# Kernel optimization log

Measured on AMD Instinct MI355X. Metric: run time of the kernel, lower is better.

## Reference

```python
import jax, jax.numpy as jnp
import numpy as np
import math

B, L, D, E, H = 8, 128, 512, 64, 8
SLOPE = 0.2
EPS = 1e-5


def setup_inputs() -> dict:
    key = jax.random.key(0)
    ks = jax.random.split(key, 10)
    s = 0.02
    x = jax.random.normal(ks[0], (B, L, D), jnp.float32)
    adj = jax.random.randint(ks[1], (B, L, L), 0, 2, jnp.int32)  # 0/1 adjacency
    e = jax.random.normal(ks[2], (B, L, L, E), jnp.float32)
    Wq = jax.random.normal(ks[3], (D, D), jnp.float32) * s
    Wkv = jax.random.normal(ks[4], (D, D), jnp.float32) * s
    We = jax.random.normal(ks[5], (E, D), jnp.float32) * s
    Wf = jax.random.normal(ks[6], (D, D), jnp.float32) * s
    bf = jnp.zeros((D,), jnp.float32)
    gamma = jnp.ones((D,), jnp.float32)
    beta = jnp.zeros((D,), jnp.float32)
    return {"x": x, "adj": adj, "e": e, "Wq": Wq, "Wkv": Wkv, "We": We,
            "Wf": Wf, "bf": bf, "gamma": gamma, "beta": beta}


def reference(x, adj, e, Wq, Wkv, We, Wf, bf, gamma, beta):
    C = D // H
    # projections
    q = (x @ Wq).reshape(B, L, H, C).transpose(0, 2, 1, 3)    # (B,H,L,C)
    kv = (x @ Wkv).reshape(B, L, H, C).transpose(0, 2, 1, 3)  # (B,H,L,C)
    ee = (e @ We).reshape(B, L, L, H, C).transpose(0, 3, 1, 2, 4)  # (B,H,Lq,Lk,C)
    # edge-modulated value/key: depends on both query and key position
    kve = kv[:, :, None, :, :] + ee                            # (B,H,Lq,Lk,C)
    # scores
    alpha = jnp.einsum('bhqc,bhqkc->bhqk', q, kve) / math.sqrt(C)
    alpha = jax.nn.leaky_relu(alpha, SLOPE)
    mask = (adj != 0)[:, None, :, :]                           # (B,1,Lq,Lk)
    alpha = jnp.where(mask, alpha, jnp.float32(-1e9))
    alpha = jax.nn.softmax(alpha, axis=-1)                     # over keys
    # weighted sum of edge-modulated values
    out = jnp.einsum('bhqk,bhqkc->bhqc', alpha, kve)           # (B,H,L,C)
    out = out.transpose(0, 2, 1, 3).reshape(B, L, D)
    # FFN: Linear -> LayerNorm -> ReLU
    out = out @ Wf + bf
    mu = out.mean(-1, keepdims=True)
    var = ((out - mu) ** 2).mean(-1, keepdims=True)
    out = (out - mu) / jnp.sqrt(var + EPS) * gamma + beta
    return jax.nn.relu(out)
```

## Files before the change

kernel.cpp:

```cpp
#include <hip/hip_runtime.h>
#include <hip/hip_bf16.h>
#include <math.h>

#define BB 8
#define LL 128
#define DD 512
#define EE 64
#define HH 8
#define CC 64
#define SLOPE 0.2f
#define EPS 1e-5f

typedef short bf16x8v __attribute__((ext_vector_type(8)));
typedef float f32x4v __attribute__((ext_vector_type(4)));

static __device__ __forceinline__ unsigned short f2bf(float f) {
    union { float f; unsigned u; } v; v.f = f;
    unsigned r = v.u + 0x7FFFu + ((v.u >> 16) & 1u);
    return (unsigned short)(r >> 16);
}

static __device__ __forceinline__ bf16x8v ld8f_bf(const float* __restrict__ p) {
    const float4 v0 = *(const float4*)p;
    const float4 v1 = *(const float4*)(p + 4);
    bf16x8v r;
    r[0] = (short)f2bf(v0.x); r[1] = (short)f2bf(v0.y);
    r[2] = (short)f2bf(v0.z); r[3] = (short)f2bf(v0.w);
    r[4] = (short)f2bf(v1.x); r[5] = (short)f2bf(v1.y);
    r[6] = (short)f2bf(v1.z); r[7] = (short)f2bf(v1.w);
    return r;
}

__global__ __launch_bounds__(256) void pack_all(
    const float* __restrict__ x, const float* __restrict__ Wq,
    const float* __restrict__ Wkv, const float* __restrict__ Wf,
    const float* __restrict__ We,
    unsigned short* __restrict__ xb, unsigned short* __restrict__ Wqkv_t,
    unsigned short* __restrict__ Wf_t, unsigned short* __restrict__ We_bf,
    unsigned short* __restrict__ WeT_bf)
{
    const int blk = blockIdx.x, tid = threadIdx.x;
    if (blk < 256) {
        const int j = blk * 512 + tid * 2;
        #pragma unroll
        for (int i = 0; i < 2; ++i) {
            const float4 v = ((const float4*)x)[j + i];
            ushort4 u; u.x = f2bf(v.x); u.y = f2bf(v.y); u.z = f2bf(v.z); u.w = f2bf(v.w);
            ((ushort4*)xb)[j + i] = u;
        }
    } else if (blk < 1024) {
        __shared__ float tile[32][33];
        const int matId = (blk - 256) >> 8;
        const int t = (blk - 256) & 255;
        const float* src = matId == 0 ? Wq : (matId == 1 ? Wkv : Wf);
        unsigned short* dst = matId == 0 ? Wqkv_t : (matId == 1 ? Wqkv_t + DD * DD : Wf_t);
        const int xx = tid & 31, yy = tid >> 5;
        const int r0 = (t >> 4) * 32, c0 = (t & 15) * 32;
        #pragma unroll
        for (int j = 0; j < 32; j += 8)
            tile[yy + j][xx] = src[(r0 + yy + j) * DD + c0 + xx];
        __syncthreads();
        #pragma unroll
        for (int j = 0; j < 32; j += 8)
            dst[(c0 + yy + j) * DD + r0 + xx] = f2bf(tile[xx][yy + j]);
    } else if (blk < 1040) {
        const int j = (blk - 1024) * 512 + tid * 2;
        #pragma unroll
        for (int i = 0; i < 2; ++i) {
            const float4 v = ((const float4*)We)[j + i];
            ushort4 u; u.x = f2bf(v.x); u.y = f2bf(v.y); u.z = f2bf(v.z); u.w = f2bf(v.w);
            ((ushort4*)We_bf)[j + i] = u;
        }
    } else if (blk < 1072) {
        __shared__ float tile[32][33];
        const int t = blk - 1040;
        const int xx = tid & 31, yy = tid >> 5;
        const int r0 = (t >> 4) * 32, c0 = (t & 15) * 32;
        #pragma unroll
        for (int j = 0; j < 32; j += 8)
            tile[yy + j][xx] = We[(r0 + yy + j) * DD + c0 + xx];
        __syncthreads();
        #pragma unroll
        for (int j = 0; j < 32; j += 8)
            WeT_bf[(c0 + yy + j) * EE + r0 + xx] = f2bf(tile[xx][yy + j]);
    } else {
        const int blk2 = blk - 1072;
        const int h = blk2 >> 3;
        const int d0 = (blk2 & 7) * 64;
        const int wave = tid >> 6, lane = tid & 63;
        const int quad = lane >> 4, l16 = lane & 15;
        const int dr = d0 + wave * 16;
        f32x4v acc[4];
        #pragma unroll
        for (int t = 0; t < 4; ++t) acc[t] = (f32x4v){0.f,0.f,0.f,0.f};
        #pragma unroll
        for (int ks = 0; ks < 2; ++ks) {
            const bf16x8v a = ld8f_bf(Wq + (dr + l16) * DD + h * CC + quad * 8 + ks * 32);
            #pragma unroll
            for (int t = 0; t < 4; ++t) {
                const bf16x8v bb = ld8f_bf(We + (t * 16 + l16) * DD + h * CC + quad * 8 + ks * 32);
                acc[t] = __builtin_amdgcn_mfma_f32_16x16x32_bf16(a, bb, acc[t], 0, 0, 0);
            }
        }
        #pragma unroll
        for (int t = 0; t < 4; ++t) {
            const int nrow = 1024 + h * CC + t * 16 + l16;
            #pragma unroll
            for (int r = 0; r < 4; ++r)
                Wqkv_t[nrow * DD + dr + quad * 4 + r] = f2bf(acc[t][r]);
        }
    }
}

__global__ __launch_bounds__(256) void proj_gemm(
    const unsigned short* __restrict__ A, const unsigned short* __restrict__ Bm,
    unsigned short* __restrict__ Q_bf, unsigned short* __restrict__ KV_bf,
    unsigned short* __restrict__ KVT_bf, unsigned short* __restrict__ T_bf)
{
    const int wave = threadIdx.x >> 6, lane = threadIdx.x & 63;
    const int quad = lane >> 4, l16 = lane & 15;
    const int m0 = blockIdx.y * 64 + wave * 16;
    const int n0 = blockIdx.x * 64;
    const bf16x8v* Ap = (const bf16x8v*)(A + (m0 + l16) * DD) + quad;
    const bf16x8v* Bp = (const bf16x8v*)(Bm + (n0 + l16) * DD) + quad;
    f32x4v acc0 = {0.f,0.f,0.f,0.f}, acc1 = acc0, acc2 = acc0, acc3 = acc0;
    #pragma unroll 4
    for (int k = 0; k < 16; ++k) {
        const bf16x8v a = Ap[k * 4];
        acc0 = __builtin_amdgcn_mfma_f32_16x16x32_bf16(a, Bp[k * 4       ], acc0, 0, 0, 0);
        acc1 = __builtin_amdgcn_mfma_f32_16x16x32_bf16(a, Bp[k * 4 + 1024], acc1, 0, 0, 0);
        acc2 = __builtin_amdgcn_mfma_f32_16x16x32_bf16(a, Bp[k * 4 + 2048], acc2, 0, 0, 0);
        acc3 = __builtin_amdgcn_mfma_f32_16x16x32_bf16(a, Bp[k * 4 + 3072], acc3, 0, 0, 0);
    }
    const f32x4v accs[4] = {acc0, acc1, acc2, acc3};
    const int gm0 = m0 + quad * 4;
    #pragma unroll
    for (int t = 0; t < 4; ++t) {
        const int gn = n0 + t * 16 + l16;
        const int mat = gn >> 9, d = gn & 511, h = d >> 6, c = d & 63;
        ushort4 pk;
        pk.x = f2bf(accs[t][0]); pk.y = f2bf(accs[t][1]);
        pk.z = f2bf(accs[t][2]); pk.w = f2bf(accs[t][3]);
        unsigned short* dst = mat == 0 ? Q_bf : (mat == 1 ? KV_bf : T_bf);
        dst[(gm0 + 0) * DD + d] = pk.x;
        dst[(gm0 + 1) * DD + d] = pk.y;
        dst[(gm0 + 2) * DD + d] = pk.z;
        dst[(gm0 + 3) * DD + d] = pk.w;
        if (mat == 1) {
            const int b = gm0 >> 7, l0 = gm0 & 127;
            *(ushort4*)&KVT_bf[(((b * HH + h) * CC + c) << 7) + l0] = pk;
        }
    }
}

__global__ __launch_bounds__(256) void qk_s1(
    const unsigned short* __restrict__ Q_bf, const unsigned short* __restrict__ KV_bf,
    float* __restrict__ S1)
{
    const int wave = threadIdx.x >> 6, lane = threadIdx.x & 63;
    const int quad = lane >> 4, l16 = lane & 15;
    const int bid = blockIdx.x;
    const int batch = bid >> 3;
    const int sub = bid & 7;
    const int b = batch >> 3, h = batch & 7;
    const int q0 = (sub >> 1) * 32 + (wave >> 1) * 16;
    const int k0 = (sub & 1) * 64 + (wave & 1) * 32;
    f32x4v acc[2];
    acc[0] = (f32x4v){0.f,0.f,0.f,0.f}; acc[1] = acc[0];
    const unsigned short* Ap = Q_bf + (b * LL + q0 + l16) * DD + h * CC + quad * 8;
    #pragma unroll
    for (int ks = 0; ks < 2; ++ks) {
        const bf16x8v a = *(const bf16x8v*)(Ap + ks * 32);
        #pragma unroll
        for (int t = 0; t < 2; ++t) {
            const bf16x8v bb = *(const bf16x8v*)(KV_bf + (b * LL + k0 + t * 16 + l16) * DD + h * CC + quad * 8 + ks * 32);
            acc[t] = __builtin_amdgcn_mfma_f32_16x16x32_bf16(a, bb, acc[t], 0, 0, 0);
        }
    }
    #pragma unroll
    for (int t = 0; t < 2; ++t)
        #pragma unroll
        for (int r = 0; r < 4; ++r)
            S1[((batch * LL + q0 + quad * 4 + r) << 7) + k0 + t * 16 + l16] = acc[t][r];
}

#define ES 72
#define ETS 138
__global__ __launch_bounds__(256) void attn_fused(
    const float* __restrict__ e, const int* __restrict__ adj,
    const float* __restrict__ S1, const unsigned short* __restrict__ T_bf,
    unsigned short* __restrict__ P1, unsigned short* __restrict__ G_bf)
{
    __shared__ unsigned short lds_e[LL * ES];
    __shared__ unsigned short lds_eT[EE * ETS];
    __shared__ float s_lds[HH * 132];
    __shared__ unsigned short p_bf[HH * ETS];

    const int bq = blockIdx.x;
    const int b = bq >> 7, q = bq & 127;
    const int tid = threadIdx.x;
    const int wave = tid >> 6, lane = tid & 63, quad = lane >> 4, l16 = lane & 15;

    const float4* e4 = (const float4*)(e + (size_t)bq * (LL * EE));
    #pragma unroll
    for (int rep = 0; rep < 8; ++rep) {
        const int j = rep * 256 + tid;
        const float4 v = e4[j];
        const int k = j >> 4, x0 = (j & 15) * 4;
        ushort4 u; u.x = f2bf(v.x); u.y = f2bf(v.y); u.z = f2bf(v.z); u.w = f2bf(v.w);
        *(ushort4*)&lds_e[k * ES + x0] = u;
        lds_eT[(x0    ) * ETS + k] = u.x;
        lds_eT[(x0 + 1) * ETS + k] = u.y;
        lds_eT[(x0 + 2) * ETS + k] = u.z;
        lds_eT[(x0 + 3) * ETS + k] = u.w;
    }
    __syncthreads();

    const int hh = l16 < 8 ? l16 : 7;
    const unsigned short* Trow = T_bf + bq * DD + hh * CC + quad * 8;
    const bf16x8v tb0 = *(const bf16x8v*)(Trow);
    const bf16x8v tb1 = *(const bf16x8v*)(Trow + 32);
    f32x4v sacc[2];
    #pragma unroll
    for (int mt = 0; mt < 2; ++mt) {
        sacc[mt] = (f32x4v){0.f,0.f,0.f,0.f};
        const int kb = wave * 32 + mt * 16;
        const bf16x8v a0 = *(const bf16x8v*)&lds_e[(kb + l16) * ES + quad * 8];
        const bf16x8v a1 = *(const bf16x8v*)&lds_e[(kb + l16) * ES + 32 + quad * 8];
        sacc[mt] = __builtin_amdgcn_mfma_f32_16x16x32_bf16(a0, tb0, sacc[mt], 0, 0, 0);
        sacc[mt] = __builtin_amdgcn_mfma_f32_16x16x32_bf16(a1, tb1, sacc[mt], 0, 0, 0);
    }
    if (l16 < 8) {
        #pragma unroll
        for (int mt = 0; mt < 2; ++mt) {
            const int kk0 = wave * 32 + mt * 16 + quad * 4;
            const float4 s1v = *(const float4*)&S1[(((b * HH + l16) * LL + q) << 7) + kk0];
            const int4 av = *(const int4*)&adj[bq * LL + kk0];
            float sv[4] = {s1v.x, s1v.y, s1v.z, s1v.w};
            const int am[4] = {av.x, av.y, av.z, av.w};
            float4 o;
            float* op = (float*)&o;
            #pragma unroll
            for (int r = 0; r < 4; ++r) {
                float sc = (sv[r] + sacc[mt][r]) * 0.125f;
                sc = (sc >= 0.f) ? sc : SLOPE * sc;
                op[r] = (am[r] == 0) ? -1e9f : sc;
            }
            *(float4*)&s_lds[l16 * 132 + kk0] = o;
        }
    }
    __syncthreads();

    {
        const int h = tid >> 5, t5 = tid & 31;
        float m = -INFINITY;
        #pragma unroll
        for (int i = 0; i < 4; ++i) m = fmaxf(m, s_lds[h * 132 + t5 + i * 32]);
        #pragma unroll
        for (int off = 16; off > 0; off >>= 1) m = fmaxf(m, __shfl_down(m, off, 32));
        m = __shfl(m, 0, 32);
        const int k0 = t5 * 4;
        float ev[4];
        #pragma unroll
        for (int i = 0; i < 4; ++i) ev[i] = __expf(s_lds[h * 132 + k0 + i] - m);
        float l = ev[0] + ev[1] + ev[2] + ev[3];
        #pragma unroll
        for (int off = 16; off > 0; off >>= 1) l += __shfl_down(l, off, 32);
        l = __shfl(l, 0, 32);
        const float inv = 1.f / l;
        ushort4 pk;
        pk.x = f2bf(ev[0] * inv); pk.y = f2bf(ev[1] * inv);
        pk.z = f2bf(ev[2] * inv); pk.w = f2bf(ev[3] * inv);
        *(ushort4*)&p_bf[h * ETS + k0] = pk;
        *(ushort4*)&P1[(((b * HH + h) * LL + q) << 7) + k0] = pk;
    }
    __syncthreads();

    {
        const int hr = l16 < 8 ? l16 : 0;
        f32x4v g = {0.f,0.f,0.f,0.f};
        #pragma unroll
        for (int ks = 0; ks < 4; ++ks) {
            const bf16x8v a  = *(const bf16x8v*)&p_bf[hr * ETS + ks * 32 + quad * 8];
            const bf16x8v bb = *(const bf16x8v*)&lds_eT[(wave * 16 + l16) * ETS + ks * 32 + quad * 8];
            g = __builtin_amdgcn_mfma_f32_16x16x32_bf16(a, bb, g, 0, 0, 0);
        }
        if (quad < 2) {
            #pragma unroll
            for (int r = 0; r < 4; ++r)
                G_bf[bq * DD + (quad * 4 + r) * CC + wave * 16 + l16] = f2bf(g[r]);
        }
    }
}

__global__ __launch_bounds__(256) void pv_o2_gemm(
    const unsigned short* __restrict__ P1, const unsigned short* __restrict__ KVT_bf,
    const unsigned short* __restrict__ G_bf, const unsigned short* __restrict__ WeT_bf,
    unsigned short* __restrict__ attn_bf)
{
    const int wave = threadIdx.x >> 6, lane = threadIdx.x & 63;
    const int quad = lane >> 4, l16 = lane & 15;
    const int batch = blockIdx.x >> 2;
    const int qt = blockIdx.x & 3;
    const int q0 = qt * 32 + (wave >> 1) * 16;
    const int c0 = (wave & 1) * 32;
    const int b = batch >> 3, h = batch & 7;
    f32x4v acc[2];
    acc[0] = (f32x4v){0.f,0.f,0.f,0.f}; acc[1] = acc[0];

    const unsigned short* Ap = P1 + ((batch * LL + q0 + l16) << 7) + quad * 8;
    #pragma unroll
    for (int ks = 0; ks < 4; ++ks) {
        const bf16x8v a = *(const bf16x8v*)(Ap + ks * 32);
        #pragma unroll
        for (int t = 0; t < 2; ++t) {
            const bf16x8v bb = *(const bf16x8v*)(KVT_bf + ((batch * CC + c0 + t * 16 + l16) << 7) + quad * 8 + ks * 32);
            acc[t] = __builtin_amdgcn_mfma_f32_16x16x32_bf16(a, bb, acc[t], 0, 0, 0);
        }
    }

    const int gm = b * LL + q0;
    const unsigned short* Gp = G_bf + (gm + l16) * DD + h * CC + quad * 8;
    #pragma unroll
    for (int ks = 0; ks < 2; ++ks) {
        const bf16x8v a = *(const bf16x8v*)(Gp + ks * 32);
        #pragma unroll
        for (int t = 0; t < 2; ++t) {
            const bf16x8v bb = *(const bf16x8v*)(WeT_bf + (h * CC + c0 + t * 16 + l16) * EE + quad * 8 + ks * 32);
            acc[t] = __builtin_amdgcn_mfma_f32_16x16x32_bf16(a, bb, acc[t], 0, 0, 0);
        }
    }

    #pragma unroll
    for (int t = 0; t < 2; ++t) {
        const int d = h * CC + c0 + t * 16 + l16;
        #pragma unroll
        for (int r = 0; r < 4; ++r)
            attn_bf[(gm + quad * 4 + r) * DD + d] = f2bf(acc[t][r]);
    }
}

__global__ __launch_bounds__(256) void ffn_gemm(
    const unsigned short* __restrict__ A, const unsigned short* __restrict__ Bm,
    const float* __restrict__ bfv, float* __restrict__ vals)
{
    const int wave = threadIdx.x >> 6, lane = threadIdx.x & 63;
    const int quad = lane >> 4, l16 = lane & 15;
    const int m0 = blockIdx.y * 32 + (wave >> 1) * 16;
    const int n0 = blockIdx.x * 64 + (wave & 1) * 32;
    const bf16x8v* Ap = (const bf16x8v*)(A + (m0 + l16) * DD) + quad;
    const bf16x8v* Bp = (const bf16x8v*)(Bm + (n0 + l16) * DD) + quad;
    f32x4v acc0 = {0.f,0.f,0.f,0.f}, acc1 = acc0;
    #pragma unroll 4
    for (int k = 0; k < 16; ++k) {
        const bf16x8v a = Ap[k * 4];
        acc0 = __builtin_amdgcn_mfma_f32_16x16x32_bf16(a, Bp[k * 4       ], acc0, 0, 0, 0);
        acc1 = __builtin_amdgcn_mfma_f32_16x16x32_bf16(a, Bp[k * 4 + 1024], acc1, 0, 0, 0);
    }
    const f32x4v accs[2] = {acc0, acc1};
    #pragma unroll
    for (int t = 0; t < 2; ++t) {
        const int gn = n0 + t * 16 + l16;
        const float bias = bfv[gn];
        #pragma unroll
        for (int r = 0; r < 4; ++r)
            vals[(m0 + quad * 4 + r) * DD + gn] = accs[t][r] + bias;
    }
}

__global__ __launch_bounds__(256) void ln_kernel(
    const float* __restrict__ vals, const float* __restrict__ gamma,
    const float* __restrict__ beta, float* __restrict__ out)
{
    __shared__ float red[8];
    __shared__ float stats[2];
    const int row = blockIdx.x;
    const int tid = threadIdx.x;
    const float v0 = vals[row * DD + tid];
    const float v1 = vals[row * DD + tid + 256];
    float ls = v0 + v1;
    float lss = v0 * v0 + v1 * v1;
    #pragma unroll
    for (int off = 32; off > 0; off >>= 1) {
        ls += __shfl_down(ls, off);
        lss += __shfl_down(lss, off);
    }
    const int wid = tid >> 6;
    if ((tid & 63) == 0) { red[wid * 2] = ls; red[wid * 2 + 1] = lss; }
    __syncthreads();
    if (tid == 0) {
        float ts = 0.f, tss = 0.f;
        for (int w = 0; w < 4; ++w) { ts += red[w * 2]; tss += red[w * 2 + 1]; }
        const float mu = ts / (float)DD;
        const float var = tss / (float)DD - mu * mu;
        stats[0] = mu;
        stats[1] = rsqrtf(var + EPS);
    }
    __syncthreads();
    const float mu = stats[0], rsig = stats[1];
    const float o0 = (v0 - mu) * rsig * gamma[tid] + beta[tid];
    const float o1 = (v1 - mu) * rsig * gamma[tid + 256] + beta[tid + 256];
    out[row * DD + tid] = fmaxf(o0, 0.f);
    out[row * DD + tid + 256] = fmaxf(o1, 0.f);
}

extern "C" void kernel_launch(void* const* d_in, const int* in_sizes, int n_in,
                              void* d_out, int out_size, void* d_ws, size_t ws_size,
                              hipStream_t stream)
{
    const float* x    = (const float*)d_in[0];
    const int*   adj  = (const int*)  d_in[1];
    const float* e    = (const float*)d_in[2];
    const float* Wq   = (const float*)d_in[3];
    const float* Wkv  = (const float*)d_in[4];
    const float* We   = (const float*)d_in[5];
    const float* Wf   = (const float*)d_in[6];
    const float* bf   = (const float*)d_in[7];
    const float* gam  = (const float*)d_in[8];
    const float* bet  = (const float*)d_in[9];
    float* out = (float*)d_out;

    const int MROW = BB * LL;
    char* w = (char*)d_ws;
    unsigned short* Q_bf   = (unsigned short*)(w);
    unsigned short* KV_bf  = (unsigned short*)(w + (1u  << 20));
    unsigned short* KVT_bf = (unsigned short*)(w + (2u  << 20));
    float*          S1     = (float*)         (w + (3u  << 20));
    unsigned short* T_bf   = (unsigned short*)(w + (7u  << 20));
    unsigned short* P1     = (unsigned short*)(w + (8u  << 20));
    unsigned short* G_bf   = (unsigned short*)(w + (10u << 20));
    float*          vals   = (float*)         (w + (11u << 20));
    unsigned short* xb     = (unsigned short*)(w + (13u << 20));
    unsigned short* Wqkv_t = (unsigned short*)(w + (14u << 20));
    unsigned short* Wf_t   = (unsigned short*)(w + (15u << 20) + (512u << 10));
    unsigned short* We_bf  = (unsigned short*)(w + (16u << 20));
    unsigned short* WeT_bf = (unsigned short*)(w + (16u << 20) + (64u << 10));

    pack_all<<<1136, 256, 0, stream>>>(x, Wq, Wkv, Wf, We, xb, Wqkv_t, Wf_t, We_bf, WeT_bf);
    proj_gemm<<<dim3(24, 16), 256, 0, stream>>>(xb, Wqkv_t, Q_bf, KV_bf, KVT_bf, T_bf);
    qk_s1<<<512, 256, 0, stream>>>(Q_bf, KV_bf, S1);
    attn_fused<<<MROW, 256, 0, stream>>>(e, adj, S1, T_bf, P1, G_bf);
    pv_o2_gemm<<<256, 256, 0, stream>>>(P1, KVT_bf, G_bf, WeT_bf, (unsigned short*)Q_bf);
    ffn_gemm<<<dim3(8, 32), 256, 0, stream>>>((unsigned short*)Q_bf, Wf_t, bf, vals);
    ln_kernel<<<MROW, 256, 0, stream>>>(vals, gam, bet, out);
}
```

Baseline: 141.0 us.

## Fuse all stages into one cooperative persistent kernel with grid syncs

Replaces seven separate kernel launches with a single cooperative persistent kernel that loops over virtual blocks per stage and uses grid.sync between stages. Shared memory is unioned across stages. It also drops the unused We_bf pack and gives attn output its own buffer. This is meant to remove launch overhead and inter-kernel gaps. The cost is grid-wide barriers, occupancy limited by the largest shared-memory footprint, and a grid capped at 1024 blocks. If the cooperative launch fails, it falls back to the separate kernels.

```diff
diff --git a/kernel.cpp b/kernel.cpp
--- a/kernel.cpp
+++ b/kernel.cpp
@@ -1,6 +1,9 @@
 #include <hip/hip_runtime.h>
+#include <hip/hip_cooperative_groups.h>
 #include <hip/hip_bf16.h>
 #include <math.h>
+
+namespace cg = cooperative_groups;
 
 #define BB 8
 #define LL 128
@@ -10,6 +13,10 @@
 #define CC 64
 #define SLOPE 0.2f
 #define EPS 1e-5f
+
+#define ES 72
+#define ETS 138
+#define NPACK 1120
 
 typedef short bf16x8v __attribute__((ext_vector_type(8)));
 typedef float f32x4v __attribute__((ext_vector_type(4)));
@@ -31,15 +38,23 @@
     return r;
 }
 
-__global__ __launch_bounds__(256) void pack_all(
+struct AttnSmem {
+    unsigned short lds_e[LL * ES];
+    unsigned short lds_eT[EE * ETS];
+    float s_lds[HH * 132];
+    unsigned short p_bf[HH * ETS];
+};
+struct LnSmem { float red[8]; float stats[2]; };
+
+
+__device__ __forceinline__ void pack_body(int blk, int tid,
     const float* __restrict__ x, const float* __restrict__ Wq,
     const float* __restrict__ Wkv, const float* __restrict__ Wf,
     const float* __restrict__ We,
     unsigned short* __restrict__ xb, unsigned short* __restrict__ Wqkv_t,
-    unsigned short* __restrict__ Wf_t, unsigned short* __restrict__ We_bf,
-    unsigned short* __restrict__ WeT_bf)
-{
-    const int blk = blockIdx.x, tid = threadIdx.x;
+    unsigned short* __restrict__ Wf_t, unsigned short* __restrict__ WeT_bf,
+    float (*tile)[33])
+{
     if (blk < 256) {
         const int j = blk * 512 + tid * 2;
         #pragma unroll
@@ -49,7 +64,6 @@
             ((ushort4*)xb)[j + i] = u;
         }
     } else if (blk < 1024) {
-        __shared__ float tile[32][33];
         const int matId = (blk - 256) >> 8;
         const int t = (blk - 256) & 255;
         const float* src = matId == 0 ? Wq : (matId == 1 ? Wkv : Wf);
@@ -63,17 +77,8 @@
         #pragma unroll
         for (int j = 0; j < 32; j += 8)
             dst[(c0 + yy + j) * DD + r0 + xx] = f2bf(tile[xx][yy + j]);
-    } else if (blk < 1040) {
-        const int j = (blk - 1024) * 512 + tid * 2;
-        #pragma unroll
-        for (int i = 0; i < 2; ++i) {
-            const float4 v = ((const float4*)We)[j + i];
-            ushort4 u; u.x = f2bf(v.x); u.y = f2bf(v.y); u.z = f2bf(v.z); u.w = f2bf(v.w);
-            ((ushort4*)We_bf)[j + i] = u;
-        }
-    } else if (blk < 1072) {
-        __shared__ float tile[32][33];
-        const int t = blk - 1040;
+    } else if (blk < 1056) {
+        const int t = blk - 1024;
         const int xx = tid & 31, yy = tid >> 5;
         const int r0 = (t >> 4) * 32, c0 = (t & 15) * 32;
         #pragma unroll
@@ -84,7 +89,7 @@
         for (int j = 0; j < 32; j += 8)
             WeT_bf[(c0 + yy + j) * EE + r0 + xx] = f2bf(tile[xx][yy + j]);
     } else {
-        const int blk2 = blk - 1072;
+        const int blk2 = blk - 1056;
         const int h = blk2 >> 3;
         const int d0 = (blk2 & 7) * 64;
         const int wave = tid >> 6, lane = tid & 63;
@@ -112,15 +117,15 @@
     }
 }
 
-__global__ __launch_bounds__(256) void proj_gemm(
+__device__ __forceinline__ void proj_body(int vb, int tid,
     const unsigned short* __restrict__ A, const unsigned short* __restrict__ Bm,
     unsigned short* __restrict__ Q_bf, unsigned short* __restrict__ KV_bf,
     unsigned short* __restrict__ KVT_bf, unsigned short* __restrict__ T_bf)
 {
-    const int wave = threadIdx.x >> 6, lane = threadIdx.x & 63;
+    const int wave = tid >> 6, lane = tid & 63;
     const int quad = lane >> 4, l16 = lane & 15;
-    const int m0 = blockIdx.y * 64 + wave * 16;
-    const int n0 = blockIdx.x * 64;
+    const int m0 = (vb / 24) * 64 + wave * 16;
+    const int n0 = (vb % 24) * 64;
     const bf16x8v* Ap = (const bf16x8v*)(A + (m0 + l16) * DD) + quad;
     const bf16x8v* Bp = (const bf16x8v*)(Bm + (n0 + l16) * DD) + quad;
     f32x4v acc0 = {0.f,0.f,0.f,0.f}, acc1 = acc0, acc2 = acc0, acc3 = acc0;
@@ -153,15 +158,14 @@
     }
 }
 
-__global__ __launch_bounds__(256) void qk_s1(
+__device__ __forceinline__ void qk_body(int vb, int tid,
     const unsigned short* __restrict__ Q_bf, const unsigned short* __restrict__ KV_bf,
     float* __restrict__ S1)
 {
-    const int wave = threadIdx.x >> 6, lane = threadIdx.x & 63;
+    const int wave = tid >> 6, lane = tid & 63;
     const int quad = lane >> 4, l16 = lane & 15;
-    const int bid = blockIdx.x;
-    const int batch = bid >> 3;
-    const int sub = bid & 7;
+    const int batch = vb >> 3;
+    const int sub = vb & 7;
     const int b = batch >> 3, h = batch & 7;
     const int q0 = (sub >> 1) * 32 + (wave >> 1) * 16;
     const int k0 = (sub & 1) * 64 + (wave & 1) * 32;
@@ -184,21 +188,12 @@
             S1[((batch * LL + q0 + quad * 4 + r) << 7) + k0 + t * 16 + l16] = acc[t][r];
 }
 
-#define ES 72
-#define ETS 138
-__global__ __launch_bounds__(256) void attn_fused(
+__device__ __forceinline__ void attn_body(int bq, int tid, AttnSmem* sm,
     const float* __restrict__ e, const int* __restrict__ adj,
     const float* __restrict__ S1, const unsigned short* __restrict__ T_bf,
     unsigned short* __restrict__ P1, unsigned short* __restrict__ G_bf)
 {
-    __shared__ unsigned short lds_e[LL * ES];
-    __shared__ unsigned short lds_eT[EE * ETS];
-    __shared__ float s_lds[HH * 132];
-    __shared__ unsigned short p_bf[HH * ETS];
-
-    const int bq = blockIdx.x;
     const int b = bq >> 7, q = bq & 127;
-    const int tid = threadIdx.x;
     const int wave = tid >> 6, lane = tid & 63, quad = lane >> 4, l16 = lane & 15;
 
     const float4* e4 = (const float4*)(e + (size_t)bq * (LL * EE));
@@ -208,11 +203,11 @@
         const float4 v = e4[j];
         const int k = j >> 4, x0 = (j & 15) * 4;
         ushort4 u; u.x = f2bf(v.x); u.y = f2bf(v.y); u.z = f2bf(v.z); u.w = f2bf(v.w);
-        *(ushort4*)&lds_e[k * ES + x0] = u;
-        lds_eT[(x0    ) * ETS + k] = u.x;
-        lds_eT[(x0 + 1) * ETS + k] = u.y;
-        lds_eT[(x0 + 2) * ETS + k] = u.z;
-        lds_eT[(x0 + 3) * ETS + k] = u.w;
+        *(ushort4*)&sm->lds_e[k * ES + x0] = u;
+        sm->lds_eT[(x0    ) * ETS + k] = u.x;
+        sm->lds_eT[(x0 + 1) * ETS + k] = u.y;
+        sm->lds_eT[(x0 + 2) * ETS + k] = u.z;
+        sm->lds_eT[(x0 + 3) * ETS + k] = u.w;
     }
     __syncthreads();
 
@@ -225,8 +220,8 @@
     for (int mt = 0; mt < 2; ++mt) {
         sacc[mt] = (f32x4v){0.f,0.f,0.f,0.f};
         const int kb = wave * 32 + mt * 16;
-        const bf16x8v a0 = *(const bf16x8v*)&lds_e[(kb + l16) * ES + quad * 8];
-        const bf16x8v a1 = *(const bf16x8v*)&lds_e[(kb + l16) * ES + 32 + quad * 8];
+        const bf16x8v a0 = *(const bf16x8v*)&sm->lds_e[(kb + l16) * ES + quad * 8];
+        const bf16x8v a1 = *(const bf16x8v*)&sm->lds_e[(kb + l16) * ES + 32 + quad * 8];
         sacc[mt] = __builtin_amdgcn_mfma_f32_16x16x32_bf16(a0, tb0, sacc[mt], 0, 0, 0);
         sacc[mt] = __builtin_amdgcn_mfma_f32_16x16x32_bf16(a1, tb1, sacc[mt], 0, 0, 0);
     }
@@ -246,7 +241,7 @@
                 sc = (sc >= 0.f) ? sc : SLOPE * sc;
                 op[r] = (am[r] == 0) ? -1e9f : sc;
             }
-            *(float4*)&s_lds[l16 * 132 + kk0] = o;
+            *(float4*)&sm->s_lds[l16 * 132 + kk0] = o;
         }
     }
     __syncthreads();
@@ -255,14 +250,14 @@
         const int h = tid >> 5, t5 = tid & 31;
         float m = -INFINITY;
         #pragma unroll
-        for (int i = 0; i < 4; ++i) m = fmaxf(m, s_lds[h * 132 + t5 + i * 32]);
+        for (int i = 0; i < 4; ++i) m = fmaxf(m, sm->s_lds[h * 132 + t5 + i * 32]);
         #pragma unroll
         for (int off = 16; off > 0; off >>= 1) m = fmaxf(m, __shfl_down(m, off, 32));
         m = __shfl(m, 0, 32);
         const int k0 = t5 * 4;
         float ev[4];
         #pragma unroll
-        for (int i = 0; i < 4; ++i) ev[i] = __expf(s_lds[h * 132 + k0 + i] - m);
+        for (int i = 0; i < 4; ++i) ev[i] = __expf(sm->s_lds[h * 132 + k0 + i] - m);
         float l = ev[0] + ev[1] + ev[2] + ev[3];
         #pragma unroll
         for (int off = 16; off > 0; off >>= 1) l += __shfl_down(l, off, 32);
@@ -271,7 +266,7 @@
         ushort4 pk;
         pk.x = f2bf(ev[0] * inv); pk.y = f2bf(ev[1] * inv);
         pk.z = f2bf(ev[2] * inv); pk.w = f2bf(ev[3] * inv);
-        *(ushort4*)&p_bf[h * ETS + k0] = pk;
+        *(ushort4*)&sm->p_bf[h * ETS + k0] = pk;
         *(ushort4*)&P1[(((b * HH + h) * LL + q) << 7) + k0] = pk;
     }
     __syncthreads();
@@ -281,8 +276,8 @@
         f32x4v g = {0.f,0.f,0.f,0.f};
         #pragma unroll
         for (int ks = 0; ks < 4; ++ks) {
-            const bf16x8v a  = *(const bf16x8v*)&p_bf[hr * ETS + ks * 32 + quad * 8];
-            const bf16x8v bb = *(const bf16x8v*)&lds_eT[(wave * 16 + l16) * ETS + ks * 32 + quad * 8];
+            const bf16x8v a  = *(const bf16x8v*)&sm->p_bf[hr * ETS + ks * 32 + quad * 8];
+            const bf16x8v bb = *(const bf16x8v*)&sm->lds_eT[(wave * 16 + l16) * ETS + ks * 32 + quad * 8];
             g = __builtin_amdgcn_mfma_f32_16x16x32_bf16(a, bb, g, 0, 0, 0);
         }
         if (quad < 2) {
@@ -293,15 +288,15 @@
     }
 }
 
-__global__ __launch_bounds__(256) void pv_o2_gemm(
+__device__ __forceinline__ void pv_body(int vb, int tid,
     const unsigned short* __restrict__ P1, const unsigned short* __restrict__ KVT_bf,
     const unsigned short* __restrict__ G_bf, const unsigned short* __restrict__ WeT_bf,
     unsigned short* __restrict__ attn_bf)
 {
-    const int wave = threadIdx.x >> 6, lane = threadIdx.x & 63;
+    const int wave = tid >> 6, lane = tid & 63;
     const int quad = lane >> 4, l16 = lane & 15;
-    const int batch = blockIdx.x >> 2;
-    const int qt = blockIdx.x & 3;
+    const int batch = vb >> 2;
+    const int qt = vb & 3;
     const int q0 = qt * 32 + (wave >> 1) * 16;
     const int c0 = (wave & 1) * 32;
     const int b = batch >> 3, h = batch & 7;
@@ -318,7 +313,6 @@
             acc[t] = __builtin_amdgcn_mfma_f32_16x16x32_bf16(a, bb, acc[t], 0, 0, 0);
         }
     }
-
     const int gm = b * LL + q0;
     const unsigned short* Gp = G_bf + (gm + l16) * DD + h * CC + quad * 8;
     #pragma unroll
@@ -330,7 +324,6 @@
             acc[t] = __builtin_amdgcn_mfma_f32_16x16x32_bf16(a, bb, acc[t], 0, 0, 0);
         }
     }
-
     #pragma unroll
     for (int t = 0; t < 2; ++t) {
         const int d = h * CC + c0 + t * 16 + l16;
@@ -340,14 +333,14 @@
     }
 }
 
-__global__ __launch_bounds__(256) void ffn_gemm(
+__device__ __forceinline__ void ffn_body(int vb, int tid,
     const unsigned short* __restrict__ A, const unsigned short* __restrict__ Bm,
     const float* __restrict__ bfv, float* __restrict__ vals)
 {
-    const int wave = threadIdx.x >> 6, lane = threadIdx.x & 63;
+    const int wave = tid >> 6, lane = tid & 63;
     const int quad = lane >> 4, l16 = lane & 15;
-    const int m0 = blockIdx.y * 32 + (wave >> 1) * 16;
-    const int n0 = blockIdx.x * 64 + (wave & 1) * 32;
+    const int m0 = (vb >> 3) * 32 + (wave >> 1) * 16;
+    const int n0 = (vb & 7) * 64 + (wave & 1) * 32;
     const bf16x8v* Ap = (const bf16x8v*)(A + (m0 + l16) * DD) + quad;
     const bf16x8v* Bp = (const bf16x8v*)(Bm + (n0 + l16) * DD) + quad;
     f32x4v acc0 = {0.f,0.f,0.f,0.f}, acc1 = acc0;
@@ -368,14 +361,10 @@
     }
 }
 
-__global__ __launch_bounds__(256) void ln_kernel(
+__device__ __forceinline__ void ln_body(int row, int tid, LnSmem* sm,
     const float* __restrict__ vals, const float* __restrict__ gamma,
     const float* __restrict__ beta, float* __restrict__ out)
 {
-    __shared__ float red[8];
-    __shared__ float stats[2];
-    const int row = blockIdx.x;
-    const int tid = threadIdx.x;
     const float v0 = vals[row * DD + tid];
     const float v1 = vals[row * DD + tid + 256];
     float ls = v0 + v1;
@@ -386,22 +375,118 @@
         lss += __shfl_down(lss, off);
     }
     const int wid = tid >> 6;
-    if ((tid & 63) == 0) { red[wid * 2] = ls; red[wid * 2 + 1] = lss; }
+    if ((tid & 63) == 0) { sm->red[wid * 2] = ls; sm->red[wid * 2 + 1] = lss; }
     __syncthreads();
     if (tid == 0) {
         float ts = 0.f, tss = 0.f;
-        for (int w = 0; w < 4; ++w) { ts += red[w * 2]; tss += red[w * 2 + 1]; }
+        for (int w = 0; w < 4; ++w) { ts += sm->red[w * 2]; tss += sm->red[w * 2 + 1]; }
         const float mu = ts / (float)DD;
         const float var = tss / (float)DD - mu * mu;
-        stats[0] = mu;
-        stats[1] = rsqrtf(var + EPS);
+        sm->stats[0] = mu;
+        sm->stats[1] = rsqrtf(var + EPS);
     }
     __syncthreads();
-    const float mu = stats[0], rsig = stats[1];
+    const float mu = sm->stats[0], rsig = sm->stats[1];
     const float o0 = (v0 - mu) * rsig * gamma[tid] + beta[tid];
     const float o1 = (v1 - mu) * rsig * gamma[tid + 256] + beta[tid + 256];
     out[row * DD + tid] = fmaxf(o0, 0.f);
     out[row * DD + tid + 256] = fmaxf(o1, 0.f);
+}
+
+struct MegaArgs {
+    const float *x; const int *adj; const float *e;
+    const float *Wq, *Wkv, *We, *Wf, *bfv, *gam, *bet;
+    float *out;
+    unsigned short *xb, *Wqkv_t, *Wf_t, *WeT_bf;
+    unsigned short *Q_bf, *KV_bf, *KVT_bf, *T_bf, *P1, *G_bf, *attn_bf;
+    float *S1, *vals;
+};
+
+__global__ __launch_bounds__(256) void mega(MegaArgs A)
+{
+    __shared__ union SmU {
+        AttnSmem at;
+        float tile[32][33];
+        LnSmem ln;
+    } sm;
+    cg::grid_group grid = cg::this_grid();
+    const int tid = threadIdx.x;
+    const int NB = gridDim.x;
+
+    for (int vb = blockIdx.x; vb < NPACK; vb += NB) {
+        __syncthreads();
+        pack_body(vb, tid, A.x, A.Wq, A.Wkv, A.Wf, A.We,
+                  A.xb, A.Wqkv_t, A.Wf_t, A.WeT_bf, sm.tile);
+    }
+    __threadfence(); grid.sync();
+
+    for (int vb = blockIdx.x; vb < 384; vb += NB)
+        proj_body(vb, tid, A.xb, A.Wqkv_t, A.Q_bf, A.KV_bf, A.KVT_bf, A.T_bf);
+    __threadfence(); grid.sync();
+
+    for (int vb = blockIdx.x; vb < 512; vb += NB)
+        qk_body(vb, tid, A.Q_bf, A.KV_bf, A.S1);
+    __threadfence(); grid.sync();
+
+    for (int vb = blockIdx.x; vb < 1024; vb += NB) {
+        attn_body(vb, tid, &sm.at, A.e, A.adj, A.S1, A.T_bf, A.P1, A.G_bf);
+        __syncthreads();
+    }
+    __threadfence(); grid.sync();
+
+    for (int vb = blockIdx.x; vb < 256; vb += NB)
+        pv_body(vb, tid, A.P1, A.KVT_bf, A.G_bf, A.WeT_bf, A.attn_bf);
+    __threadfence(); grid.sync();
+
+    for (int vb = blockIdx.x; vb < 256; vb += NB)
+        ffn_body(vb, tid, A.attn_bf, A.Wf_t, A.bfv, A.vals);
+    __threadfence(); grid.sync();
+
+    for (int vb = blockIdx.x; vb < 1024; vb += NB)
+        ln_body(vb, tid, &sm.ln, A.vals, A.gam, A.bet, A.out);
+}
+
+__global__ __launch_bounds__(256) void pack_k(
+    const float* x, const float* Wq, const float* Wkv, const float* Wf, const float* We,
+    unsigned short* xb, unsigned short* Wqkv_t, unsigned short* Wf_t, unsigned short* WeT_bf)
+{
+    __shared__ float tile[32][33];
+    pack_body(blockIdx.x, threadIdx.x, x, Wq, Wkv, Wf, We, xb, Wqkv_t, Wf_t, WeT_bf, tile);
+}
+__global__ __launch_bounds__(256) void proj_k(
+    const unsigned short* A, const unsigned short* Bm, unsigned short* Q_bf,
+    unsigned short* KV_bf, unsigned short* KVT_bf, unsigned short* T_bf)
+{
+    proj_body(blockIdx.x, threadIdx.x, A, Bm, Q_bf, KV_bf, KVT_bf, T_bf);
+}
+__global__ __launch_bounds__(256) void qk_k(
+    const unsigned short* Q_bf, const unsigned short* KV_bf, float* S1)
+{
+    qk_body(blockIdx.x, threadIdx.x, Q_bf, KV_bf, S1);
+}
+__global__ __launch_bounds__(256) void attn_k(
+    const float* e, const int* adj, const float* S1, const unsigned short* T_bf,
+    unsigned short* P1, unsigned short* G_bf)
+{
+    __shared__ AttnSmem s;
+    attn_body(blockIdx.x, threadIdx.x, &s, e, adj, S1, T_bf, P1, G_bf);
+}
+__global__ __launch_bounds__(256) void pv_k(
+    const unsigned short* P1, const unsigned short* KVT_bf, const unsigned short* G_bf,
+    const unsigned short* WeT_bf, unsigned short* attn_bf)
+{
+    pv_body(blockIdx.x, threadIdx.x, P1, KVT_bf, G_bf, WeT_bf, attn_bf);
+}
+__global__ __launch_bounds__(256) void ffn_k(
+    const unsigned short* A, const unsigned short* Bm, const float* bfv, float* vals)
+{
+    ffn_body(blockIdx.x, threadIdx.x, A, Bm, bfv, vals);
+}
+__global__ __launch_bounds__(256) void ln_k(
+    const float* vals, const float* gamma, const float* beta, float* out)
+{
+    __shared__ LnSmem s;
+    ln_body(blockIdx.x, threadIdx.x, &s, vals, gamma, beta, out);
 }
 
 extern "C" void kernel_launch(void* const* d_in, const int* in_sizes, int n_in,
@@ -420,27 +505,58 @@
     const float* bet  = (const float*)d_in[9];
     float* out = (float*)d_out;
 
-    const int MROW = BB * LL;
     char* w = (char*)d_ws;
-    unsigned short* Q_bf   = (unsigned short*)(w);
-    unsigned short* KV_bf  = (unsigned short*)(w + (1u  << 20));
-    unsigned short* KVT_bf = (unsigned short*)(w + (2u  << 20));
-    float*          S1     = (float*)         (w + (3u  << 20));
-    unsigned short* T_bf   = (unsigned short*)(w + (7u  << 20));
-    unsigned short* P1     = (unsigned short*)(w + (8u  << 20));
-    unsigned short* G_bf   = (unsigned short*)(w + (10u << 20));
-    float*          vals   = (float*)         (w + (11u << 20));
-    unsigned short* xb     = (unsigned short*)(w + (13u << 20));
-    unsigned short* Wqkv_t = (unsigned short*)(w + (14u << 20));
-    unsigned short* Wf_t   = (unsigned short*)(w + (15u << 20) + (512u << 10));
-    unsigned short* We_bf  = (unsigned short*)(w + (16u << 20));
-    unsigned short* WeT_bf = (unsigned short*)(w + (16u << 20) + (64u << 10));
-
-    pack_all<<<1136, 256, 0, stream>>>(x, Wq, Wkv, Wf, We, xb, Wqkv_t, Wf_t, We_bf, WeT_bf);
-    proj_gemm<<<dim3(24, 16), 256, 0, stream>>>(xb, Wqkv_t, Q_bf, KV_bf, KVT_bf, T_bf);
-    qk_s1<<<512, 256, 0, stream>>>(Q_bf, KV_bf, S1);
-    attn_fused<<<MROW, 256, 0, stream>>>(e, adj, S1, T_bf, P1, G_bf);
-    pv_o2_gemm<<<256, 256, 0, stream>>>(P1, KVT_bf, G_bf, WeT_bf, (unsigned short*)Q_bf);
-    ffn_gemm<<<dim3(8, 32), 256, 0, stream>>>((unsigned short*)Q_bf, Wf_t, bf, vals);
-    ln_kernel<<<MROW, 256, 0, stream>>>(vals, gam, bet, out);
-}
+    unsigned short* Q_bf    = (unsigned short*)(w);
+    unsigned short* KV_bf   = (unsigned short*)(w + (1u  << 20));
+    unsigned short* KVT_bf  = (unsigned short*)(w + (2u  << 20));
+    float*          S1      = (float*)         (w + (3u  << 20));
+    unsigned short* T_bf    = (unsigned short*)(w + (7u  << 20));
+    unsigned short* P1      = (unsigned short*)(w + (8u  << 20));
+    unsigned short* G_bf    = (unsigned short*)(w + (10u << 20));
+    unsigned short* attn_bf = (unsigned short*)(w + (11u << 20));
+    float*          vals    = (float*)         (w + (12u << 20));
+    unsigned short* xb      = (unsigned short*)(w + (14u << 20));
+    unsigned short* Wqkv_t  = (unsigned short*)(w + (15u << 20));
+    unsigned short* Wf_t    = (unsigned short*)(w + (16u << 20) + (512u << 10));
+    unsigned short* WeT_bf  = (unsigned short*)(w + (17u << 20));
+
+    MegaArgs ma;
+    ma.x = x; ma.adj = adj; ma.e = e;
+    ma.Wq = Wq; ma.Wkv = Wkv; ma.We = We; ma.Wf = Wf;
+    ma.bfv = bf; ma.gam = gam; ma.bet = bet;
+    ma.out = out;
+    ma.xb = xb; ma.Wqkv_t = Wqkv_t; ma.Wf_t = Wf_t; ma.WeT_bf = WeT_bf;
+    ma.Q_bf = Q_bf; ma.KV_bf = KV_bf; ma.KVT_bf = KVT_bf; ma.T_bf = T_bf;
+    ma.P1 = P1; ma.G_bf = G_bf; ma.attn_bf = attn_bf;
+    ma.S1 = S1; ma.vals = vals;
+
+    static int s_grid = 0;
+    if (s_grid == 0) {
+        int nb = 0;
+        hipError_t qe = hipOccupancyMaxActiveBlocksPerMultiprocessor(&nb, mega, 256, 0);
+        if (qe != hipSuccess || nb < 1) {
+            s_grid = -1;
+        } else {
+            long g = (long)nb * 256;
+            if (g > 1024) g = 1024;
+            s_grid = (int)g;
+        }
+    }
+
+    bool done = false;
+    if (s_grid > 0) {
+        void* kargs[] = { (void*)&ma };
+        hipError_t err = hipLaunchCooperativeKernel(mega, dim3(s_grid), dim3(256),
+                                                    kargs, 0u, stream);
+        done = (err == hipSuccess);
+    }
+    if (!done) {
+        pack_k<<<NPACK, 256, 0, stream>>>(x, Wq, Wkv, Wf, We, xb, Wqkv_t, Wf_t, WeT_bf);
+        proj_k<<<384, 256, 0, stream>>>(xb, Wqkv_t, Q_bf, KV_bf, KVT_bf, T_bf);
+        qk_k<<<512, 256, 0, stream>>>(Q_bf, KV_bf, S1);
+        attn_k<<<1024, 256, 0, stream>>>(e, adj, S1, T_bf, P1, G_bf);
+        pv_k<<<256, 256, 0, stream>>>(P1, KVT_bf, G_bf, WeT_bf, attn_bf);
+        ffn_k<<<256, 256, 0, stream>>>(attn_bf, Wf_t, bf, vals);
+        ln_k<<<1024, 256, 0, stream>>>(vals, gam, bet, out);
+    }
+}
```

Result: slower. 515.3 us (+265.4%).
